# Optimization experiments

Measured on AMD Instinct MI355X. Metric: run time of the kernel, lower is better.

Reference implementation:

```python
import jax, jax.numpy as jnp
import numpy as np

B, L, D, H, NLAYERS = 32, 2048, 1024, 16, 4
HD = D // H
NEG = -1e30


def setup_inputs() -> dict:
    key = jax.random.key(0)
    ks = jax.random.split(key, 12)
    tokens = jax.random.normal(ks[0], (B, L, D), dtype=jnp.float32)
    lengths = jax.random.randint(ks[1], (B,), 1, L + 1, dtype=jnp.int32)
    query_token = jax.random.normal(ks[2], (1, D), dtype=jnp.float32)
    s = 0.02
    Wq = jax.random.normal(ks[3], (NLAYERS, D, D), dtype=jnp.float32) * s
    Wk = jax.random.normal(ks[4], (NLAYERS, D, D), dtype=jnp.float32) * s
    Wv = jax.random.normal(ks[5], (NLAYERS, D, D), dtype=jnp.float32) * s
    Wo = jax.random.normal(ks[6], (NLAYERS, D, D), dtype=jnp.float32) * s
    bq = jnp.zeros((NLAYERS, D), jnp.float32)
    bk = jnp.zeros((NLAYERS, D), jnp.float32)
    bv = jnp.zeros((NLAYERS, D), jnp.float32)
    bo = jnp.zeros((NLAYERS, D), jnp.float32)
    gamma = jnp.ones((NLAYERS, D), jnp.float32)
    beta = jnp.zeros((NLAYERS, D), jnp.float32)
    return dict(tokens=tokens, lengths=lengths, query_token=query_token,
                Wq=Wq, bq=bq, Wk=Wk, bk=bk, Wv=Wv, bv=bv, Wo=Wo, bo=bo,
                gamma=gamma, beta=beta)


def _layernorm(x, g, b):
    mu = jnp.mean(x, axis=-1, keepdims=True)
    var = jnp.mean(jnp.square(x - mu), axis=-1, keepdims=True)
    return (x - mu) * jax.lax.rsqrt(var + 1e-5) * g + b


def reference(tokens, lengths, query_token, Wq, bq, Wk, bk, Wv, bv, Wo, bo, gamma, beta):
    # valid[b, l] = True where token l exists (inverse of key_padding_mask)
    valid = jnp.arange(L)[None, :] < lengths[:, None]            # [B, L]
    scale = 1.0 / jnp.sqrt(jnp.float32(HD))
    # zero out padded positions like the torch padded buffer (math-neutral)
    toks = tokens * valid[:, :, None].astype(tokens.dtype)       # [B, L, D]
    q = jnp.broadcast_to(query_token[None], (B, 1, D))           # [B, 1, D]
    for i in range(NLAYERS):
        qh = (q @ Wq[i] + bq[i]).reshape(B, 1, H, HD)            # [B, 1, H, hd]
        kh = (toks @ Wk[i] + bk[i]).reshape(B, L, H, HD)         # [B, L, H, hd]
        vh = (toks @ Wv[i] + bv[i]).reshape(B, L, H, HD)
        scores = jnp.einsum('bqhd,bkhd->bhqk', qh, kh) * scale   # [B, H, 1, L]
        scores = jnp.where(valid[:, None, None, :], scores, NEG)
        attn = jax.nn.softmax(scores, axis=-1)
        out = jnp.einsum('bhqk,bkhd->bqhd', attn, vh).reshape(B, 1, D)
        out = out @ Wo[i] + bo[i]
        q = _layernorm(out, gamma[i], beta[i])
    return q[:, 0, :]                                            # [B, D]
```

## Files before the change

kernel.cpp:

```cpp
#include <hip/hip_runtime.h>
#include <hip/hip_bf16.h>
#include <cstdint>
#include <cstddef>

#define BB 32
#define LL 2048
#define DD 1024
#define HH 16
#define HDIM 64
#define NL 4
#define NCHUNK 8
#define CHUNK 256
#define NEGINF -1e30f
#define KS 32
#define KLEN 32

typedef __attribute__((ext_vector_type(8))) short bf16x8;
typedef __attribute__((ext_vector_type(4))) float f32x4;

__device__ __forceinline__ unsigned short f2b(float x) {
    union { float f; unsigned int u; } v; v.f = x;
    unsigned int r = (v.u + 0x7FFFu + ((v.u >> 16) & 1u)) >> 16;
    return (unsigned short)r;
}

__global__ __launch_bounds__(256) void k_bcast(const float* __restrict__ qt,
        float* __restrict__ g0) {
    int i = blockIdx.x * 256 + threadIdx.x;
    g0[i] = qt[i & (DD - 1)];
}

template<int SRC>
__global__ __launch_bounds__(256) void k_gemv(
        const float* __restrict__ Xg,
        const float* __restrict__ stats, const float* __restrict__ gamma,
        const float* __restrict__ beta,
        const float* __restrict__ parts_in, const float* __restrict__ bias_in,
        const float* __restrict__ ctx_p, const float* __restrict__ m_p,
        const float* __restrict__ s_p,
        const float* __restrict__ W, float* __restrict__ outp) {
    int bid = blockIdx.x, tid = threadIdx.x;
    int ct = bid & 15, ks = bid >> 4;
    int e0 = ks * KLEN;
    __shared__ float Xs[BB][KLEN];
    __shared__ float wgtS[BB][NCHUNK];
    __shared__ float mgS[BB], SgS[BB];
    if (SRC == 3) {
        if (tid < BB) {
            int b = tid; float m = NEGINF;
            for (int c8 = 0; c8 < NCHUNK; ++c8)
                m = fmaxf(m, m_p[(b * NCHUNK + c8) * HH + ct]);
            float S = 0.f;
            for (int c8 = 0; c8 < NCHUNK; ++c8)
                S += s_p[(b * NCHUNK + c8) * HH + ct] *
                     __expf(m_p[(b * NCHUNK + c8) * HH + ct] - m);
            mgS[b] = m; SgS[b] = S;
        }
        __syncthreads();
        {
            int b = tid >> 3, c8 = tid & 7;
            wgtS[b][c8] = __expf(m_p[(b * NCHUNK + c8) * HH + ct] - mgS[b]) / SgS[b];
        }
        __syncthreads();
    }
#pragma unroll
    for (int j = 0; j < 4; ++j) {
        int i = tid + j * 256;
        int b = i >> 5, k = i & 31;
        float x;
        if (SRC == 0) {
            x = Xg[(size_t)b * DD + e0 + k];
        } else if (SRC == 1) {
            float mu = stats[b * 2], rstd = stats[b * 2 + 1];
            x = (Xg[(size_t)b * DD + e0 + k] - mu) * rstd * gamma[e0 + k] + beta[e0 + k];
        } else if (SRC == 2) {
            x = bias_in[e0 + k];
#pragma unroll
            for (int j2 = 0; j2 < KS; ++j2)
                x += parts_in[((size_t)(j2 * BB) + b) * DD + e0 + k];
        } else {
            x = 0.f;
#pragma unroll
            for (int c8 = 0; c8 < NCHUNK; ++c8)
                x += wgtS[b][c8] *
                     ctx_p[(((size_t)(b * NCHUNK + c8)) * HH + ct) * DD + e0 + k];
        }
        Xs[b][k] = x;
    }
    __syncthreads();
    int col = tid & 63, bg = tid >> 6;
    int c = ct * 64 + col;
    float acc[8] = {0.f, 0.f, 0.f, 0.f, 0.f, 0.f, 0.f, 0.f};
    for (int k = 0; k < KLEN; k += 4) {
        float w0 = W[(size_t)(e0 + k) * DD + c];
        float w1 = W[(size_t)(e0 + k + 1) * DD + c];
        float w2 = W[(size_t)(e0 + k + 2) * DD + c];
        float w3 = W[(size_t)(e0 + k + 3) * DD + c];
#pragma unroll
        for (int bb = 0; bb < 8; ++bb) {
            const float4 xv = *(const float4*)&Xs[bg * 8 + bb][k];
            acc[bb] += xv.x * w0 + xv.y * w1 + xv.z * w2 + xv.w * w3;
        }
    }
#pragma unroll
    for (int bb = 0; bb < 8; ++bb)
        outp[((size_t)(ks * BB) + bg * 8 + bb) * DD + c] = acc[bb];
}

__global__ __launch_bounds__(256) void k_comb_bias(const float* __restrict__ parts,
        const float* __restrict__ bias, float* __restrict__ Y) {
    int i = blockIdx.x * 256 + threadIdx.x;
    int b = i >> 10, c = i & (DD - 1);
    float v = bias[c];
#pragma unroll
    for (int ks = 0; ks < KS; ++ks)
        v += parts[((size_t)(ks * BB) + b) * DD + c];
    Y[i] = v;
}

__global__ __launch_bounds__(256) void k_stats(const float* __restrict__ parts,
        const float* __restrict__ bo, float* __restrict__ oraw,
        float* __restrict__ stats) {
    int b = blockIdx.x, tid = threadIdx.x;
    float s1 = 0.f, s2 = 0.f;
#pragma unroll
    for (int j = 0; j < 4; ++j) {
        int c = tid + j * 256;
        float v = bo[c];
#pragma unroll
        for (int ks = 0; ks < KS; ++ks)
            v += parts[((size_t)(ks * BB) + b) * DD + c];
        oraw[(size_t)b * DD + c] = v;
        s1 += v; s2 += v * v;
    }
#pragma unroll
    for (int off = 32; off; off >>= 1) {
        s1 += __shfl_xor(s1, off);
        s2 += __shfl_xor(s2, off);
    }
    __shared__ float r1[4], r2[4];
    int w = tid >> 6;
    if ((tid & 63) == 0) { r1[w] = s1; r2[w] = s2; }
    __syncthreads();
    if (tid == 0) {
        float a = r1[0] + r1[1] + r1[2] + r1[3];
        float q = r2[0] + r2[1] + r2[2] + r2[3];
        float mu = a / (float)DD, var = q / (float)DD - mu * mu;
        stats[b * 2] = mu;
        stats[b * 2 + 1] = rsqrtf(var + 1e-5f);
    }
}

__global__ __launch_bounds__(256) void k_final(const float* __restrict__ oraw,
        const float* __restrict__ stats, const float* __restrict__ gamma,
        const float* __restrict__ beta, float* __restrict__ outp) {
    int i = blockIdx.x * 256 + threadIdx.x;
    int b = i >> 10, c = i & (DD - 1);
    outp[i] = (oraw[i] - stats[b * 2]) * stats[b * 2 + 1] * gamma[c] + beta[c];
}

__global__ __launch_bounds__(256) void k_wk(const float* __restrict__ qh,
        const float* __restrict__ Wk, const float* __restrict__ bk,
        unsigned short* __restrict__ wk16, float* __restrict__ sb) {
    int h = blockIdx.x >> 4, et = blockIdx.x & 15;
    int tid = threadIdx.x;
    __shared__ float qs[BB][HDIM + 1];
    for (int i = tid; i < BB * HDIM; i += 256) {
        int bb = i >> 6, d = i & 63;
        qs[bb][d] = qh[bb * DD + h * HDIM + d];
    }
    __syncthreads();
    int b = tid & 31, eo = tid >> 5;
    for (int k = 0; k < 8; ++k) {
        int e = et * 64 + eo * 8 + k;
        const float* wrow = Wk + (size_t)e * DD + h * HDIM;
        float acc = 0.f;
#pragma unroll
        for (int d = 0; d < HDIM; ++d) acc += qs[b][d] * wrow[d];
        wk16[((size_t)(b * HH + h)) * DD + e] = f2b(acc);
    }
    if (et == 0 && tid < BB) {
        float acc = 0.f;
#pragma unroll
        for (int d = 0; d < HDIM; ++d) acc += qs[tid][d] * bk[h * HDIM + d];
        sb[tid * HH + h] = acc;
    }
}

template<int MODE>
__global__ __launch_bounds__(1024) void k_attn(const float* __restrict__ toks,
        unsigned short* __restrict__ tcache,
        const int* __restrict__ lens, const unsigned short* __restrict__ wk16,
        const float* __restrict__ sb, float* __restrict__ ctx_p,
        float* __restrict__ m_p, float* __restrict__ s_p) {
    int b = blockIdx.x >> 3, chunk = blockIdx.x & 7;
    int tid = threadIdx.x, lane = tid & 63, w = tid >> 6;
    int len = lens[b];
    int base = chunk * CHUNK;
    int pidx = (b * NCHUNK + chunk) * HH;
    if (base >= len) {
        if (tid < HH) { m_p[pidx + tid] = NEGINF; s_p[pidx + tid] = 0.f; }
        return;
    }
    int nv = min(CHUNK, len - base);

    __shared__ __align__(16) unsigned short Tr[32][1032];
    __shared__ float Sred[16][HH][34];
    __shared__ unsigned short Pt[HH][40];
    __shared__ float sm_m[HH], sm_s[HH], sm_c[HH];

    if (tid < HH) { sm_m[tid] = NEGINF; sm_s[tid] = 0.f; }

    int hq = lane & 15, qg = lane >> 4;
    const unsigned short* wkb = wk16 + ((size_t)(b * HH + hq)) * DD + w * 64 + 8 * qg;
    bf16x8 afr0 = *(const bf16x8*)(wkb);
    bf16x8 afr1 = *(const bf16x8*)(wkb + 32);
    f32x4 zer = {0.f, 0.f, 0.f, 0.f};
    f32x4 ctxacc[4] = {zer, zer, zer, zer};
    float sbh = (tid < 512) ? sb[b * HH + (tid >> 5)] : 0.f;
    int st = tid >> 7;
    int se = (tid & 127) * 8;
    __syncthreads();

    for (int g = 0; g < 8; ++g) {
        int t0 = g * 32;
        if (t0 >= nv) break;
        if (MODE == 2) {
            const unsigned short* srcr = tcache + ((size_t)(b * LL + base + t0)) * DD;
#pragma unroll
            for (int p = 0; p < 4; ++p) {
                int t = p * 8 + st;
                bf16x8 v = *(const bf16x8*)(srcr + (size_t)t * DD + se);
                *(bf16x8*)&Tr[t][se] = v;
            }
        } else {
            const float* srcr = toks + ((size_t)(b * LL + base + t0)) * DD;
#pragma unroll
            for (int p = 0; p < 4; ++p) {
                int t = p * 8 + st;
                const float* sp = srcr + (size_t)t * DD + se;
                float4 a0 = *(const float4*)sp;
                float4 a1 = *(const float4*)(sp + 4);
                bf16x8 v;
                v[0] = f2b(a0.x); v[1] = f2b(a0.y); v[2] = f2b(a0.z); v[3] = f2b(a0.w);
                v[4] = f2b(a1.x); v[5] = f2b(a1.y); v[6] = f2b(a1.z); v[7] = f2b(a1.w);
                *(bf16x8*)&Tr[t][se] = v;
                if (MODE == 1)
                    *(bf16x8*)(tcache + ((size_t)(b * LL + base + t0 + t)) * DD + se) = v;
            }
        }
        __syncthreads();
        f32x4 s0 = zer, s1 = zer;
        {
            int eb = w * 64 + 8 * qg;
            s0 = __builtin_amdgcn_mfma_f32_16x16x32_bf16(afr0, *(const bf16x8*)&Tr[hq][eb], s0, 0, 0, 0);
            s0 = __builtin_amdgcn_mfma_f32_16x16x32_bf16(afr1, *(const bf16x8*)&Tr[hq][eb + 32], s0, 0, 0, 0);
            s1 = __builtin_amdgcn_mfma_f32_16x16x32_bf16(afr0, *(const bf16x8*)&Tr[16 + hq][eb], s1, 0, 0, 0);
            s1 = __builtin_amdgcn_mfma_f32_16x16x32_bf16(afr1, *(const bf16x8*)&Tr[16 + hq][eb + 32], s1, 0, 0, 0);
        }
#pragma unroll
        for (int r = 0; r < 4; ++r) {
            Sred[w][qg * 4 + r][hq] = s0[r];
            Sred[w][qg * 4 + r][16 + hq] = s1[r];
        }
        __syncthreads();
        if (tid < 512) {
            int h = tid >> 5, t = tid & 31;
            float s = 0.f;
#pragma unroll
            for (int ww = 0; ww < 16; ++ww) s += Sred[ww][h][t];
            s = (s + sbh) * 0.125f;
            bool valid = (t0 + t) < nv;
            if (!valid) s = NEGINF;
            float tm = s;
#pragma unroll
            for (int off = 16; off; off >>= 1) tm = fmaxf(tm, __shfl_xor(tm, off, 32));
            float oldm = sm_m[h];
            float newm = fmaxf(oldm, tm);
            float pv = valid ? __expf(s - newm) : 0.f;
            float ps = pv;
#pragma unroll
            for (int off = 16; off; off >>= 1) ps += __shfl_xor(ps, off, 32);
            if (t == 0) {
                float corr = __expf(oldm - newm);
                sm_c[h] = corr;
                sm_m[h] = newm;
                sm_s[h] = sm_s[h] * corr + ps;
            }
            Pt[h][t] = f2b(pv);
        }
        __syncthreads();
        {
            float cr[4];
#pragma unroll
            for (int r = 0; r < 4; ++r) cr[r] = sm_c[qg * 4 + r];
            bf16x8 pafr;
            ushort4 pa0 = *(const ushort4*)&Pt[hq][8 * qg];
            ushort4 pa1 = *(const ushort4*)&Pt[hq][8 * qg + 4];
            pafr[0] = pa0.x; pafr[1] = pa0.y; pafr[2] = pa0.z; pafr[3] = pa0.w;
            pafr[4] = pa1.x; pafr[5] = pa1.y; pafr[6] = pa1.z; pafr[7] = pa1.w;
#pragma unroll
            for (int et = 0; et < 4; ++et) {
#pragma unroll
                for (int r = 0; r < 4; ++r) ctxacc[et][r] *= cr[r];
                bf16x8 bfr;
                int ec = w * 64 + et * 16 + hq;
#pragma unroll
                for (int i = 0; i < 8; ++i) bfr[i] = (short)Tr[8 * qg + i][ec];
                ctxacc[et] = __builtin_amdgcn_mfma_f32_16x16x32_bf16(pafr, bfr, ctxacc[et], 0, 0, 0);
            }
        }
        __syncthreads();
    }
    if (tid < HH) { m_p[pidx + tid] = sm_m[tid]; s_p[pidx + tid] = sm_s[tid]; }
#pragma unroll
    for (int et = 0; et < 4; ++et)
#pragma unroll
        for (int r = 0; r < 4; ++r) {
            int h = qg * 4 + r, e = w * 64 + et * 16 + hq;
            ctx_p[((size_t)pidx + h) * DD + e] = ctxacc[et][r];
        }
}

extern "C" void kernel_launch(void* const* d_in, const int* in_sizes, int n_in,
                              void* d_out, int out_size, void* d_ws, size_t ws_size,
                              hipStream_t stream) {
    const float* toks  = (const float*)d_in[0];
    const int*   lens  = (const int*)d_in[1];
    const float* qt    = (const float*)d_in[2];
    const float* Wq    = (const float*)d_in[3];
    const float* bq    = (const float*)d_in[4];
    const float* Wk    = (const float*)d_in[5];
    const float* bk    = (const float*)d_in[6];
    const float* Wv    = (const float*)d_in[7];
    const float* bv    = (const float*)d_in[8];
    const float* Wo    = (const float*)d_in[9];
    const float* bo    = (const float*)d_in[10];
    const float* gamma = (const float*)d_in[11];
    const float* beta  = (const float*)d_in[12];
    float* out = (float*)d_out;
    float* ws  = (float*)d_ws;

    float* ctx_p = ws;
    float* m_p   = ws + 4194304;
    float* s_p   = ws + 4198400;
    float* pvp   = ws + 4202496;
    float* op    = ws + 5251072;
    float* qp    = ws + 6299648;
    float* oraw  = ws + 7348224;
    float* stats = ws + 7380992;
    float* qh    = ws + 7381056;
    float* sbuf  = ws + 7413824;
    unsigned short* wk16 = (unsigned short*)(ws + 7414336);
    const size_t base_floats = 7676480;
    unsigned short* tcache = (unsigned short*)(ws + base_floats);
    const size_t need_cache = base_floats * 4 + (size_t)BB * LL * DD * 2;
    const bool use_cache = (ws_size >= need_cache);

    float* g0 = oraw;

    k_bcast<<<128, 256, 0, stream>>>(qt, g0);
    k_gemv<0><<<512, 256, 0, stream>>>(g0, nullptr, nullptr, nullptr, nullptr,
            nullptr, nullptr, nullptr, nullptr, Wq, qp);
    k_comb_bias<<<128, 256, 0, stream>>>(qp, bq, qh);
    k_wk<<<256, 256, 0, stream>>>(qh, Wk, bk, wk16, sbuf);

    for (int i = 0; i < NL; ++i) {
        if (use_cache) {
            if (i == 0)
                k_attn<1><<<256, 1024, 0, stream>>>(toks, tcache, lens, wk16,
                        sbuf, ctx_p, m_p, s_p);
            else
                k_attn<2><<<256, 1024, 0, stream>>>(toks, tcache, lens, wk16,
                        sbuf, ctx_p, m_p, s_p);
        } else {
            k_attn<0><<<256, 1024, 0, stream>>>(toks, tcache, lens, wk16,
                    sbuf, ctx_p, m_p, s_p);
        }
        const float* Wv_i = Wv + (size_t)i * DD * DD;
        const float* Wo_i = Wo + (size_t)i * DD * DD;
        k_gemv<3><<<512, 256, 0, stream>>>(nullptr, nullptr, nullptr, nullptr,
                nullptr, nullptr, ctx_p, m_p, s_p, Wv_i, pvp);
        k_gemv<2><<<512, 256, 0, stream>>>(nullptr, nullptr, nullptr, nullptr,
                pvp, bv + i * DD, nullptr, nullptr, nullptr, Wo_i, op);
        k_stats<<<32, 256, 0, stream>>>(op, bo + i * DD, oraw, stats);
        if (i == NL - 1) {
            k_final<<<128, 256, 0, stream>>>(oraw, stats, gamma + i * DD,
                    beta + i * DD, out);
        } else {
            k_gemv<1><<<512, 256, 0, stream>>>(oraw, stats, gamma + i * DD,
                    beta + i * DD, nullptr, nullptr, nullptr, nullptr, nullptr,
                    Wq + (size_t)(i + 1) * DD * DD, qp);
            k_comb_bias<<<128, 256, 0, stream>>>(qp, bq + (i + 1) * DD, qh);
            k_wk<<<256, 256, 0, stream>>>(qh, Wk + (size_t)(i + 1) * DD * DD,
                    bk + (i + 1) * DD, wk16, sbuf);
        }
    }
}
```

Before: 349.2 us.

## Fuse split-K reductions into consumers, drop broadcast kernel, prefetch attention tiles

```diff
diff --git a/kernel.cpp b/kernel.cpp
--- a/kernel.cpp
+++ b/kernel.cpp
@@ -12,8 +12,6 @@
 #define NCHUNK 8
 #define CHUNK 256
 #define NEGINF -1e30f
-#define KS 32
-#define KLEN 32
 
 typedef __attribute__((ext_vector_type(8))) short bf16x8;
 typedef __attribute__((ext_vector_type(4))) float f32x4;
@@ -24,13 +22,7 @@
     return (unsigned short)r;
 }
 
-__global__ __launch_bounds__(256) void k_bcast(const float* __restrict__ qt,
-        float* __restrict__ g0) {
-    int i = blockIdx.x * 256 + threadIdx.x;
-    g0[i] = qt[i & (DD - 1)];
-}
-
-template<int SRC>
+template<int SRC, int KSP>
 __global__ __launch_bounds__(256) void k_gemv(
         const float* __restrict__ Xg,
         const float* __restrict__ stats, const float* __restrict__ gamma,
@@ -39,10 +31,11 @@
         const float* __restrict__ ctx_p, const float* __restrict__ m_p,
         const float* __restrict__ s_p,
         const float* __restrict__ W, float* __restrict__ outp) {
+    constexpr int KL = DD / KSP;
     int bid = blockIdx.x, tid = threadIdx.x;
     int ct = bid & 15, ks = bid >> 4;
-    int e0 = ks * KLEN;
-    __shared__ float Xs[BB][KLEN];
+    int e0 = ks * KL;
+    __shared__ float Xs[BB][KL];
     __shared__ float wgtS[BB][NCHUNK];
     __shared__ float mgS[BB], SgS[BB];
     if (SRC == 3) {
@@ -63,20 +56,19 @@
         }
         __syncthreads();
     }
-#pragma unroll
-    for (int j = 0; j < 4; ++j) {
+    for (int j = 0; j < (BB * KL) / 256; ++j) {
         int i = tid + j * 256;
-        int b = i >> 5, k = i & 31;
+        int b = i / KL, k = i % KL;
         float x;
         if (SRC == 0) {
-            x = Xg[(size_t)b * DD + e0 + k];
+            x = Xg[e0 + k];
         } else if (SRC == 1) {
             float mu = stats[b * 2], rstd = stats[b * 2 + 1];
             x = (Xg[(size_t)b * DD + e0 + k] - mu) * rstd * gamma[e0 + k] + beta[e0 + k];
         } else if (SRC == 2) {
             x = bias_in[e0 + k];
 #pragma unroll
-            for (int j2 = 0; j2 < KS; ++j2)
+            for (int j2 = 0; j2 < 32; ++j2)
                 x += parts_in[((size_t)(j2 * BB) + b) * DD + e0 + k];
         } else {
             x = 0.f;
@@ -91,7 +83,7 @@
     int col = tid & 63, bg = tid >> 6;
     int c = ct * 64 + col;
     float acc[8] = {0.f, 0.f, 0.f, 0.f, 0.f, 0.f, 0.f, 0.f};
-    for (int k = 0; k < KLEN; k += 4) {
+    for (int k = 0; k < KL; k += 4) {
         float w0 = W[(size_t)(e0 + k) * DD + c];
         float w1 = W[(size_t)(e0 + k + 1) * DD + c];
         float w2 = W[(size_t)(e0 + k + 2) * DD + c];
@@ -107,44 +99,29 @@
         outp[((size_t)(ks * BB) + bg * 8 + bb) * DD + c] = acc[bb];
 }
 
-__global__ __launch_bounds__(256) void k_comb_bias(const float* __restrict__ parts,
-        const float* __restrict__ bias, float* __restrict__ Y) {
-    int i = blockIdx.x * 256 + threadIdx.x;
-    int b = i >> 10, c = i & (DD - 1);
-    float v = bias[c];
-#pragma unroll
-    for (int ks = 0; ks < KS; ++ks)
-        v += parts[((size_t)(ks * BB) + b) * DD + c];
-    Y[i] = v;
-}
-
-__global__ __launch_bounds__(256) void k_stats(const float* __restrict__ parts,
+__global__ __launch_bounds__(1024) void k_stats(const float* __restrict__ parts,
         const float* __restrict__ bo, float* __restrict__ oraw,
         float* __restrict__ stats) {
-    int b = blockIdx.x, tid = threadIdx.x;
-    float s1 = 0.f, s2 = 0.f;
-#pragma unroll
-    for (int j = 0; j < 4; ++j) {
-        int c = tid + j * 256;
-        float v = bo[c];
-#pragma unroll
-        for (int ks = 0; ks < KS; ++ks)
-            v += parts[((size_t)(ks * BB) + b) * DD + c];
-        oraw[(size_t)b * DD + c] = v;
-        s1 += v; s2 += v * v;
-    }
+    int b = blockIdx.x, c = threadIdx.x;
+    float v = bo[c];
+#pragma unroll
+    for (int ks = 0; ks < 8; ++ks)
+        v += parts[((size_t)(ks * BB) + b) * DD + c];
+    oraw[(size_t)b * DD + c] = v;
+    float s1 = v, s2 = v * v;
 #pragma unroll
     for (int off = 32; off; off >>= 1) {
         s1 += __shfl_xor(s1, off);
         s2 += __shfl_xor(s2, off);
     }
-    __shared__ float r1[4], r2[4];
-    int w = tid >> 6;
-    if ((tid & 63) == 0) { r1[w] = s1; r2[w] = s2; }
+    __shared__ float r1[16], r2[16];
+    int w = c >> 6;
+    if ((c & 63) == 0) { r1[w] = s1; r2[w] = s2; }
     __syncthreads();
-    if (tid == 0) {
-        float a = r1[0] + r1[1] + r1[2] + r1[3];
-        float q = r2[0] + r2[1] + r2[2] + r2[3];
+    if (c == 0) {
+        float a = 0.f, q = 0.f;
+#pragma unroll
+        for (int i = 0; i < 16; ++i) { a += r1[i]; q += r2[i]; }
         float mu = a / (float)DD, var = q / (float)DD - mu * mu;
         stats[b * 2] = mu;
         stats[b * 2 + 1] = rsqrtf(var + 1e-5f);
@@ -159,7 +136,8 @@
     outp[i] = (oraw[i] - stats[b * 2]) * stats[b * 2 + 1] * gamma[c] + beta[c];
 }
 
-__global__ __launch_bounds__(256) void k_wk(const float* __restrict__ qh,
+__global__ __launch_bounds__(256) void k_wk(const float* __restrict__ qp,
+        const float* __restrict__ bq,
         const float* __restrict__ Wk, const float* __restrict__ bk,
         unsigned short* __restrict__ wk16, float* __restrict__ sb) {
     int h = blockIdx.x >> 4, et = blockIdx.x & 15;
@@ -167,7 +145,11 @@
     __shared__ float qs[BB][HDIM + 1];
     for (int i = tid; i < BB * HDIM; i += 256) {
         int bb = i >> 6, d = i & 63;
-        qs[bb][d] = qh[bb * DD + h * HDIM + d];
+        float v = bq[h * HDIM + d];
+#pragma unroll
+        for (int ks = 0; ks < 8; ++ks)
+            v += qp[((size_t)(ks * BB + bb)) * DD + h * HDIM + d];
+        qs[bb][d] = v;
     }
     __syncthreads();
     int b = tid & 31, eo = tid >> 5;
@@ -203,6 +185,7 @@
         return;
     }
     int nv = min(CHUNK, len - base);
+    int ng = (nv + 31) >> 5;
 
     __shared__ __align__(16) unsigned short Tr[32][1032];
     __shared__ float Sred[16][HH][34];
@@ -220,35 +203,49 @@
     float sbh = (tid < 512) ? sb[b * HH + (tid >> 5)] : 0.f;
     int st = tid >> 7;
     int se = (tid & 127) * 8;
+    const size_t rowbase = (size_t)(b * LL + base);
+
+    bf16x8 pc[4];
+    float4 pa[4], pb[4];
+    auto LOADG = [&](int g) {
+        if (MODE == 2) {
+            const unsigned short* s0p = tcache + (rowbase + g * 32) * DD + se;
+#pragma unroll
+            for (int p = 0; p < 4; ++p)
+                pc[p] = *(const bf16x8*)(s0p + (size_t)(p * 8 + st) * DD);
+        } else {
+            const float* s0p = toks + (rowbase + g * 32) * DD + se;
+#pragma unroll
+            for (int p = 0; p < 4; ++p) {
+                const float* sp = s0p + (size_t)(p * 8 + st) * DD;
+                pa[p] = *(const float4*)sp;
+                pb[p] = *(const float4*)(sp + 4);
+            }
+        }
+    };
+    LOADG(0);
     __syncthreads();
 
-    for (int g = 0; g < 8; ++g) {
+    for (int g = 0; g < ng; ++g) {
         int t0 = g * 32;
-        if (t0 >= nv) break;
         if (MODE == 2) {
-            const unsigned short* srcr = tcache + ((size_t)(b * LL + base + t0)) * DD;
+#pragma unroll
+            for (int p = 0; p < 4; ++p)
+                *(bf16x8*)&Tr[p * 8 + st][se] = pc[p];
+        } else {
 #pragma unroll
             for (int p = 0; p < 4; ++p) {
-                int t = p * 8 + st;
-                bf16x8 v = *(const bf16x8*)(srcr + (size_t)t * DD + se);
-                *(bf16x8*)&Tr[t][se] = v;
+                bf16x8 v;
+                v[0] = f2b(pa[p].x); v[1] = f2b(pa[p].y);
+                v[2] = f2b(pa[p].z); v[3] = f2b(pa[p].w);
+                v[4] = f2b(pb[p].x); v[5] = f2b(pb[p].y);
+                v[6] = f2b(pb[p].z); v[7] = f2b(pb[p].w);
+                *(bf16x8*)&Tr[p * 8 + st][se] = v;
+                if (MODE == 1)
+                    *(bf16x8*)(tcache + (rowbase + t0 + p * 8 + st) * DD + se) = v;
             }
-        } else {
-            const float* srcr = toks + ((size_t)(b * LL + base + t0)) * DD;
-#pragma unroll
-            for (int p = 0; p < 4; ++p) {
-                int t = p * 8 + st;
-                const float* sp = srcr + (size_t)t * DD + se;
-                float4 a0 = *(const float4*)sp;
-                float4 a1 = *(const float4*)(sp + 4);
-                bf16x8 v;
-                v[0] = f2b(a0.x); v[1] = f2b(a0.y); v[2] = f2b(a0.z); v[3] = f2b(a0.w);
-                v[4] = f2b(a1.x); v[5] = f2b(a1.y); v[6] = f2b(a1.z); v[7] = f2b(a1.w);
-                *(bf16x8*)&Tr[t][se] = v;
-                if (MODE == 1)
-                    *(bf16x8*)(tcache + ((size_t)(b * LL + base + t0 + t)) * DD + se) = v;
-            }
-        }
+        }
+        if (g + 1 < ng) LOADG(g + 1);
         __syncthreads();
         f32x4 s0 = zer, s1 = zer;
         {
@@ -346,24 +343,19 @@
     float* s_p   = ws + 4198400;
     float* pvp   = ws + 4202496;
     float* op    = ws + 5251072;
-    float* qp    = ws + 6299648;
-    float* oraw  = ws + 7348224;
-    float* stats = ws + 7380992;
-    float* qh    = ws + 7381056;
-    float* sbuf  = ws + 7413824;
-    unsigned short* wk16 = (unsigned short*)(ws + 7414336);
-    const size_t base_floats = 7676480;
+    float* qp    = ws + 5513216;
+    float* oraw  = ws + 5775360;
+    float* stats = ws + 5808128;
+    float* sbuf  = ws + 5808192;
+    unsigned short* wk16 = (unsigned short*)(ws + 5808704);
+    const size_t base_floats = 6070848;
     unsigned short* tcache = (unsigned short*)(ws + base_floats);
     const size_t need_cache = base_floats * 4 + (size_t)BB * LL * DD * 2;
     const bool use_cache = (ws_size >= need_cache);
 
-    float* g0 = oraw;
-
-    k_bcast<<<128, 256, 0, stream>>>(qt, g0);
-    k_gemv<0><<<512, 256, 0, stream>>>(g0, nullptr, nullptr, nullptr, nullptr,
-            nullptr, nullptr, nullptr, nullptr, Wq, qp);
-    k_comb_bias<<<128, 256, 0, stream>>>(qp, bq, qh);
-    k_wk<<<256, 256, 0, stream>>>(qh, Wk, bk, wk16, sbuf);
+    k_gemv<0, 8><<<128, 256, 0, stream>>>(qt, nullptr, nullptr, nullptr,
+            nullptr, nullptr, nullptr, nullptr, nullptr, Wq, qp);
+    k_wk<<<256, 256, 0, stream>>>(qp, bq, Wk, bk, wk16, sbuf);
 
     for (int i = 0; i < NL; ++i) {
         if (use_cache) {
@@ -379,21 +371,21 @@
         }
         const float* Wv_i = Wv + (size_t)i * DD * DD;
         const float* Wo_i = Wo + (size_t)i * DD * DD;
-        k_gemv<3><<<512, 256, 0, stream>>>(nullptr, nullptr, nullptr, nullptr,
+        k_gemv<3, 32><<<512, 256, 0, stream>>>(nullptr, nullptr, nullptr, nullptr,
                 nullptr, nullptr, ctx_p, m_p, s_p, Wv_i, pvp);
-        k_gemv<2><<<512, 256, 0, stream>>>(nullptr, nullptr, nullptr, nullptr,
+        k_gemv<2, 8><<<128, 256, 0, stream>>>(nullptr, nullptr, nullptr, nullptr,
                 pvp, bv + i * DD, nullptr, nullptr, nullptr, Wo_i, op);
-        k_stats<<<32, 256, 0, stream>>>(op, bo + i * DD, oraw, stats);
+        k_stats<<<32, 1024, 0, stream>>>(op, bo + i * DD, oraw, stats);
         if (i == NL - 1) {
             k_final<<<128, 256, 0, stream>>>(oraw, stats, gamma + i * DD,
                     beta + i * DD, out);
         } else {
-            k_gemv<1><<<512, 256, 0, stream>>>(oraw, stats, gamma + i * DD,
+            k_gemv<1, 8><<<128, 256, 0, stream>>>(oraw, stats, gamma + i * DD,
                     beta + i * DD, nullptr, nullptr, nullptr, nullptr, nullptr,
                     Wq + (size_t)(i + 1) * DD * DD, qp);
-            k_comb_bias<<<128, 256, 0, stream>>>(qp, bq + (i + 1) * DD, qh);
-            k_wk<<<256, 256, 0, stream>>>(qh, Wk + (size_t)(i + 1) * DD * DD,
-                    bk + (i + 1) * DD, wk16, sbuf);
-        }
-    }
-}
+            k_wk<<<256, 256, 0, stream>>>(qp, bq + (i + 1) * DD,
+                    Wk + (size_t)(i + 1) * DD * DD, bk + (i + 1) * DD,
+                    wk16, sbuf);
+        }
+    }
+}
```

Measured after the change: 402.6 us. 1.15x slower.
